# Kernel tuning notes

Measured on AMD Instinct MI355X. Metric: run time of the kernel, lower is better.

Reference implementation:

```python
import jax, jax.numpy as jnp
import numpy as np
from jax import lax

B, T = 64, 200
NUM_C, DIM_S, SIZE_M = 2000, 128, 50


def setup_inputs() -> dict:
    key = jax.random.key(0)
    ks = jax.random.split(key, 12)
    d = {}
    d['skill'] = jax.random.randint(ks[0], (B, T), 0, NUM_C)
    d['answer'] = jax.random.randint(ks[1], (B, T), 0, 2)
    s = 1.0 / np.sqrt(DIM_S)
    d['k_emb'] = jax.random.normal(ks[2], (NUM_C + 1, DIM_S), jnp.float32)
    d['v_emb'] = jax.random.normal(ks[3], (2 * NUM_C + 1, DIM_S), jnp.float32)
    # kaiming_normal on [size_m, dim_s]: std = sqrt(2/dim_s)
    d['Mk'] = jax.random.normal(ks[4], (SIZE_M, DIM_S), jnp.float32) * np.sqrt(2.0 / DIM_S)
    d['Mv0'] = jax.random.normal(ks[5], (SIZE_M, DIM_S), jnp.float32) * np.sqrt(2.0 / DIM_S)
    d['f_W'] = jax.random.normal(ks[6], (DIM_S, 2 * DIM_S), jnp.float32) * (1.0 / np.sqrt(2 * DIM_S))
    d['f_b'] = jnp.zeros((DIM_S,), jnp.float32)
    d['p_W'] = jax.random.normal(ks[7], (NUM_C, DIM_S), jnp.float32) * s
    d['p_b'] = jnp.zeros((NUM_C,), jnp.float32)
    d['e_W'] = jax.random.normal(ks[8], (DIM_S, DIM_S), jnp.float32) * s
    d['e_b'] = jnp.zeros((DIM_S,), jnp.float32)
    d['a_W'] = jax.random.normal(ks[9], (DIM_S, DIM_S), jnp.float32) * s
    d['a_b'] = jnp.zeros((DIM_S,), jnp.float32)
    return d


def reference(skill, answer, k_emb, v_emb, Mk, Mv0, f_W, f_b, p_W, p_b, e_W, e_b, a_W, a_b):
    num_c = p_W.shape[0]
    bsz = skill.shape[0]
    answer_x = jnp.where(answer == 2, 1, answer)
    x = skill + num_c * answer_x                       # [B,T]
    k = k_emb[skill]                                   # [B,T,D]
    v = v_emb[x]                                       # [B,T,D]
    w = jax.nn.softmax(jnp.einsum('btd,md->btm', k, Mk), axis=-1)   # [B,T,M]
    e = jax.nn.sigmoid(jnp.einsum('btd,ed->bte', v, e_W) + e_b)      # [B,T,D]
    a = jnp.tanh(jnp.einsum('btd,ed->bte', v, a_W) + a_b)            # [B,T,D]

    Mv_init = jnp.broadcast_to(Mv0, (bsz,) + Mv0.shape)              # [B,M,D]

    def step(Mvt, inp):
        et, at, wt = inp                               # [B,D],[B,D],[B,M]
        # read uses pre-update memory (Mv[:, :-1] in the torch code)
        read = jnp.einsum('bm,bmd->bd', wt, Mvt)
        Mvt_new = Mvt * (1.0 - wt[:, :, None] * et[:, None, :]) + wt[:, :, None] * at[:, None, :]
        return Mvt_new, read

    _, reads = lax.scan(step, Mv_init,
                        (e.transpose(1, 0, 2), a.transpose(1, 0, 2), w.transpose(1, 0, 2)))
    reads = reads.transpose(1, 0, 2)                   # [B,T,D]

    f = jnp.tanh(jnp.concatenate([reads, k], axis=-1) @ f_W.T + f_b)  # [B,T,D]
    p = jax.nn.sigmoid(f @ p_W.T + p_b)                # [B,T,num_c] (dropout is identity at eval)
    p = p[:, :-1, :]
    next_skill = skill[:, 1:]                          # [B,T-1]
    idx = jnp.minimum(next_skill, num_c - 1)
    pred = jnp.take_along_axis(p, idx[..., None], axis=-1)[..., 0]
    pred = jnp.where(next_skill < num_c, pred, 0.0)    # index num_c -> zero row in torch one_hot
    return pred
```

## Files before the change

kernel.cpp:

```cpp
#include <hip/hip_runtime.h>
#include <math.h>

#define Bsz 64
#define Tn 200
#define NUMC 2000
#define DS 128
#define SM 50
#define NTOK (Bsz*Tn)
#define WG2 10
#define MPG2 5

typedef __attribute__((ext_vector_type(8))) short bfrag;
typedef __attribute__((ext_vector_type(4))) float f32x4;
typedef __attribute__((ext_vector_type(2))) float f32x2;
typedef __attribute__((ext_vector_type(4))) unsigned int u32x4;

__device__ __forceinline__ unsigned short f2bf(float x) {
    unsigned int u = __builtin_bit_cast(unsigned int, x);
    u = u + 0x7fffu + ((u >> 16) & 1u);
    return (unsigned short)(u >> 16);
}
__device__ __forceinline__ unsigned int pack2(float a, float b) {
    return (unsigned int)f2bf(a) | ((unsigned int)f2bf(b) << 16);
}
__device__ __forceinline__ bfrag mk_frag(f32x4 x, f32x4 y) {
    u32x4 t;
    t[0] = pack2(x[0], x[1]); t[1] = pack2(x[2], x[3]);
    t[2] = pack2(y[0], y[1]); t[3] = pack2(y[2], y[3]);
    return __builtin_bit_cast(bfrag, t);
}

__device__ __forceinline__ float fast_exp(float x)  { return __builtin_amdgcn_exp2f(x * 1.44269504f); }
__device__ __forceinline__ float fast_rcp(float x)  { return __builtin_amdgcn_rcpf(x); }
__device__ __forceinline__ float fast_sigmoid(float x) { return fast_rcp(1.f + fast_exp(-x)); }
__device__ __forceinline__ float fast_tanh(float x) { return 1.f - 2.f * fast_rcp(fast_exp(2.f * x) + 1.f); }

__device__ __forceinline__ void load_group(const bfrag* __restrict__ B, int nt0, int L, bfrag bf[4][4]) {
    #pragma unroll
    for (int t = 0; t < 4; t++)
        #pragma unroll
        for (int ki = 0; ki < 4; ki++)
            bf[t][ki] = B[(size_t)((nt0 + t) * 4 + ki) * 64 + L];
}
__device__ __forceinline__ void mfma_group(const bfrag A[4], const bfrag bf[4][4], f32x4 acc[4]) {
    #pragma unroll
    for (int ki = 0; ki < 4; ki++)
        #pragma unroll
        for (int t = 0; t < 4; t++)
            acc[t] = __builtin_amdgcn_mfma_f32_16x16x32_bf16(A[ki], bf[t][ki], acc[t], 0, 0, 0);
}

__global__ __launch_bounds__(256) void k0_cast(
    const float* __restrict__ eW, const float* __restrict__ aW,
    const float* __restrict__ fW, const float* __restrict__ Mk,
    unsigned int* __restrict__ BeaU, unsigned int* __restrict__ BkmU,
    unsigned int* __restrict__ Bf0U)
{
    const int g = blockIdx.x * 256 + threadIdx.x;
    if (g >= 9216) return;
    int gm, mat;
    unsigned int* dst;
    if (g < 4096)      { mat = 0; gm = g;        dst = BeaU; }
    else if (g < 7168) { mat = 1; gm = g - 4096; dst = BkmU; }
    else               { mat = 2; gm = g - 7168; dst = Bf0U; }
    const int nt = gm >> 8, r = gm & 255, ki = r >> 6, L = r & 63;
    const int n = nt * 16 + (L & 15);
    const int k = ki * 32 + (L >> 4) * 8;

    const float* src = nullptr;
    if (mat == 0) {
        src = (n < 128) ? (eW + (size_t)n * DS + k) : (aW + (size_t)(n - 128) * DS + k);
    } else if (mat == 1) {
        if (n < 128)           src = fW + (size_t)n * (2 * DS) + DS + k;
        else if (n < 128 + SM) src = Mk + (size_t)(n - 128) * DS + k;
    } else {
        src = fW + (size_t)n * (2 * DS) + k;
    }
    float v[8];
    #pragma unroll
    for (int j = 0; j < 8; j++) v[j] = src ? src[j] : 0.f;
    u32x4 o;
    o[0] = pack2(v[0], v[1]); o[1] = pack2(v[2], v[3]);
    o[2] = pack2(v[4], v[5]); o[3] = pack2(v[6], v[7]);
    ((u32x4*)dst)[gm] = o;
}

__global__ __launch_bounds__(64) void k1_gemm(
    const int* __restrict__ skill, const int* __restrict__ answer,
    const float* __restrict__ k_emb, const float* __restrict__ v_emb,
    const unsigned int* __restrict__ BeaU, const unsigned int* __restrict__ BkmU,
    const float* __restrict__ eB, const float* __restrict__ aB,
    float* __restrict__ w2, float* __restrict__ ea_buf, float* __restrict__ kp_buf)
{
    const int bid = blockIdx.x;
    const int L = threadIdx.x, L15 = L & 15, quad = L >> 4;

    if (bid < NTOK/16) {
        const int tok0 = bid * 16;
        const int tokA = tok0 + L15;
        const int tokD0 = tok0 + quad * 4;

        const bfrag* Bea = (const bfrag*)BeaU;
        bfrag bfA[4][4], bfB[4][4];
        load_group(Bea, 0, L, bfA);
        load_group(Bea, 4, L, bfB);

        const int s  = skill[tokA];
        const int an = answer[tokA];
        const int ax = (an == 2) ? 1 : an;
        const float* vp = v_emb + ((size_t)(s + NUMC * ax)) * DS + quad * 8;
        bfrag Vf[4];
        #pragma unroll
        for (int ki = 0; ki < 4; ki++) {
            const f32x4* a = (const f32x4*)(vp + ki * 32);
            Vf[ki] = mk_frag(a[0], a[1]);
        }

        f32x4 acc[4];
        #pragma unroll
        for (int t = 0; t < 4; t++) acc[t] = (f32x4){0.f,0.f,0.f,0.f};
        mfma_group(Vf, bfA, acc);
        load_group(Bea, 8, L, bfA);
        #pragma unroll
        for (int t = 0; t < 4; t++) {
            const int n = t * 16 + L15;
            const float bias = eB[n];
            #pragma unroll
            for (int reg = 0; reg < 4; reg++)
                ea_buf[(size_t)(tokD0 + reg) * (2*DS) + 2*n] = fast_sigmoid(acc[t][reg] + bias);
        }

        #pragma unroll
        for (int t = 0; t < 4; t++) acc[t] = (f32x4){0.f,0.f,0.f,0.f};
        mfma_group(Vf, bfB, acc);
        load_group(Bea, 12, L, bfB);
        #pragma unroll
        for (int t = 0; t < 4; t++) {
            const int n = (4 + t) * 16 + L15;
            const float bias = eB[n];
            #pragma unroll
            for (int reg = 0; reg < 4; reg++)
                ea_buf[(size_t)(tokD0 + reg) * (2*DS) + 2*n] = fast_sigmoid(acc[t][reg] + bias);
        }

        #pragma unroll
        for (int t = 0; t < 4; t++) acc[t] = (f32x4){0.f,0.f,0.f,0.f};
        mfma_group(Vf, bfA, acc);
        #pragma unroll
        for (int t = 0; t < 4; t++) {
            const int n = t * 16 + L15;
            const float bias = aB[n];
            #pragma unroll
            for (int reg = 0; reg < 4; reg++)
                ea_buf[(size_t)(tokD0 + reg) * (2*DS) + 2*n + 1] = fast_tanh(acc[t][reg] + bias);
        }

        #pragma unroll
        for (int t = 0; t < 4; t++) acc[t] = (f32x4){0.f,0.f,0.f,0.f};
        mfma_group(Vf, bfB, acc);
        #pragma unroll
        for (int t = 0; t < 4; t++) {
            const int n = (4 + t) * 16 + L15;
            const float bias = aB[n];
            #pragma unroll
            for (int reg = 0; reg < 4; reg++)
                ea_buf[(size_t)(tokD0 + reg) * (2*DS) + 2*n + 1] = fast_tanh(acc[t][reg] + bias);
        }
    } else {
        const int tok0 = (bid - NTOK/16) * 16;
        const int tokA = tok0 + L15;
        const int tokD0 = tok0 + quad * 4;

        const bfrag* Bkm = (const bfrag*)BkmU;
        bfrag bfA[4][4], bfB[4][4];
        load_group(Bkm, 0, L, bfA);
        load_group(Bkm, 4, L, bfB);

        const int s = skill[tokA];
        const float* kp = k_emb + (size_t)s * DS + quad * 8;
        bfrag Kf[4];
        #pragma unroll
        for (int ki = 0; ki < 4; ki++) {
            const f32x4* b = (const f32x4*)(kp + ki * 32);
            Kf[ki] = mk_frag(b[0], b[1]);
        }

        f32x4 acc[4];
        #pragma unroll
        for (int t = 0; t < 4; t++) acc[t] = (f32x4){0.f,0.f,0.f,0.f};
        mfma_group(Kf, bfA, acc);
        load_group(Bkm, 8, L, bfA);
        #pragma unroll
        for (int t = 0; t < 4; t++) {
            const int n = t * 16 + L15;
            #pragma unroll
            for (int reg = 0; reg < 4; reg++)
                kp_buf[(size_t)(tokD0 + reg) * DS + n] = acc[t][reg];
        }

        #pragma unroll
        for (int t = 0; t < 4; t++) acc[t] = (f32x4){0.f,0.f,0.f,0.f};
        mfma_group(Kf, bfB, acc);
        #pragma unroll
        for (int t = 0; t < 4; t++) {
            const int n = (4 + t) * 16 + L15;
            #pragma unroll
            for (int reg = 0; reg < 4; reg++)
                kp_buf[(size_t)(tokD0 + reg) * DS + n] = acc[t][reg];
        }

        #pragma unroll
        for (int t = 0; t < 4; t++) acc[t] = (f32x4){0.f,0.f,0.f,0.f};
        mfma_group(Kf, bfA, acc);
        #pragma unroll
        for (int reg = 0; reg < 4; reg++) {
            float mx = -1e30f;
            #pragma unroll
            for (int t = 0; t < 4; t++) {
                const int c = t * 16 + L15;
                if (c < SM) mx = fmaxf(mx, acc[t][reg]);
            }
            #pragma unroll
            for (int msk = 1; msk <= 8; msk <<= 1)
                mx = fmaxf(mx, __shfl_xor(mx, msk));
            float ex[4], sum = 0.f;
            #pragma unroll
            for (int t = 0; t < 4; t++) {
                const int c = t * 16 + L15;
                ex[t] = (c < SM) ? fast_exp(acc[t][reg] - mx) : 0.f;
                sum += ex[t];
            }
            #pragma unroll
            for (int msk = 1; msk <= 8; msk <<= 1)
                sum += __shfl_xor(sum, msk);
            const float inv = fast_rcp(sum);
            float* wp = w2 + (size_t)(tok0 + quad * 4 + reg) * 80;
            #pragma unroll
            for (int t = 0; t < 4; t++) {
                const int c = t * 16 + L15;
                if (c < SM) wp[(c / MPG2) * 8 + (c % MPG2)] = ex[t] * inv;
            }
        }
    }
}

__global__ __launch_bounds__(64, 2) void k2_scan(
    const float* __restrict__ w2, const float* __restrict__ ea_buf,
    const float* __restrict__ Mv0, float* __restrict__ part_buf)
{
    const int bi   = blockIdx.x;
    const int b    = bi / (2*WG2);
    const int r    = bi % (2*WG2);
    const int dh   = r / WG2;
    const int mg   = r % WG2;
    const int lane = threadIdx.x;
    const int d    = dh*64 + lane;
    const int m0   = mg * MPG2;
    const int base = b * Tn;

    float Mv[MPG2];
    #pragma unroll
    for (int m = 0; m < MPG2; m++) Mv[m] = Mv0[(size_t)(m0+m)*DS + d];

    float* pout = part_buf + (size_t)mg * NTOK * DS;

    f32x2 rea[8][2];
    float rw[8][2][MPG2];

    #define LOADST(ST, T)                                                          \
        { const int tc_ = ((T) < Tn) ? (T) : 0;                                    \
          _Pragma("unroll")                                                        \
          for (int q_ = 0; q_ < 2; q_++) {                                         \
              const int tf_ = base + tc_ + q_;                                     \
              rea[ST][q_] = *(const f32x2*)(ea_buf + (size_t)tf_*(2*DS) + 2*d);    \
              const float* wp_ = w2 + (size_t)tf_*80 + mg*8;                       \
              f32x4 w4_ = *(const f32x4*)wp_;                                      \
              rw[ST][q_][0]=w4_[0]; rw[ST][q_][1]=w4_[1];                          \
              rw[ST][q_][2]=w4_[2]; rw[ST][q_][3]=w4_[3];                          \
              rw[ST][q_][4]=wp_[4];                                               \
          } }

    #define STAGE(ST, T0)                                                          \
        { _Pragma("unroll")                                                        \
          for (int q = 0; q < 2; q++) {                                            \
              const float ev = rea[ST][q][0], av = rea[ST][q][1];                  \
              float rd = 0.f;                                                      \
              _Pragma("unroll")                                                    \
              for (int m = 0; m < MPG2; m++) {                                     \
                  const float wm = rw[ST][q][m];                                   \
                  rd = fmaf(wm, Mv[m], rd);                            \
                  Mv[m] = fmaf(-wm, fmaf(ev, Mv[m], -av), Mv[m]);      \
              }                                                                    \
              pout[(size_t)(base + (T0) + q)*DS + d] = rd;                         \
          }                                                                        \
          LOADST(ST, (T0) + 16) }

    LOADST(0, 0) LOADST(1, 2) LOADST(2, 4) LOADST(3, 6)
    LOADST(4, 8) LOADST(5, 10) LOADST(6, 12) LOADST(7, 14)

    for (int blk = 0; blk < 12; blk++) {
        const int t0 = blk * 16;
        STAGE(0, t0)      STAGE(1, t0 + 2)  STAGE(2, t0 + 4)  STAGE(3, t0 + 6)
        STAGE(4, t0 + 8)  STAGE(5, t0 + 10) STAGE(6, t0 + 12) STAGE(7, t0 + 14)
    }
    STAGE(0, 192) STAGE(1, 194) STAGE(2, 196) STAGE(3, 198)
    #undef STAGE
    #undef LOADST
}

__global__ __launch_bounds__(64) void k3_gemm(
    const float* __restrict__ part_buf, const float* __restrict__ kp_buf,
    const unsigned int* __restrict__ Bf0U, const float* __restrict__ fB,
    const float* __restrict__ pW, const float* __restrict__ pB,
    const int* __restrict__ skill, float* __restrict__ out)
{
    const int L = threadIdx.x, L15 = L & 15, quad = L >> 4;
    const int tok0 = blockIdx.x * 16;
    const int tokA = tok0 + L15;
    const int tokD0 = tok0 + quad * 4;

    const bfrag* Bf0 = (const bfrag*)Bf0U;
    bfrag bfA[4][4], bfB[4][4];
    load_group(Bf0, 0, L, bfA);
    load_group(Bf0, 4, L, bfB);

    bfrag Rf[4];
    #pragma unroll
    for (int ki = 0; ki < 4; ki++) {
        const float* p0 = part_buf + (size_t)tokA * DS + ki * 32 + quad * 8;
        f32x4 x = (f32x4){0.f,0.f,0.f,0.f}, y = (f32x4){0.f,0.f,0.f,0.f};
        #pragma unroll
        for (int g = 0; g < WG2; g++) {
            const f32x4* q4 = (const f32x4*)(p0 + (size_t)g * NTOK * DS);
            x = x + q4[0]; y = y + q4[1];
        }
        Rf[ki] = mk_frag(x, y);
    }

    float f[4][8];
    f32x4 acc[4];

    #pragma unroll
    for (int t = 0; t < 4; t++) acc[t] = (f32x4){0.f,0.f,0.f,0.f};
    mfma_group(Rf, bfA, acc);
    #pragma unroll
    for (int t = 0; t < 4; t++) {
        const int n = t * 16 + L15;
        const float fb = fB[n];
        #pragma unroll
        for (int reg = 0; reg < 4; reg++)
            f[reg][t] = fast_tanh(acc[t][reg] + kp_buf[(size_t)(tokD0 + reg) * DS + n] + fb);
    }

    #pragma unroll
    for (int t = 0; t < 4; t++) acc[t] = (f32x4){0.f,0.f,0.f,0.f};
    mfma_group(Rf, bfB, acc);
    #pragma unroll
    for (int t = 0; t < 4; t++) {
        const int n = (4 + t) * 16 + L15;
        const float fb = fB[n];
        #pragma unroll
        for (int reg = 0; reg < 4; reg++)
            f[reg][4 + t] = fast_tanh(acc[t][reg] + kp_buf[(size_t)(tokD0 + reg) * DS + n] + fb);
    }

    #pragma unroll
    for (int reg = 0; reg < 4; reg++) {
        const int tok = tokD0 + reg;
        const int t = tok % Tn;
        const bool act = (t < Tn - 1);
        int sn = 0, ix = 0;
        float contrib = 0.f;
        if (act) {
            sn = skill[tok + 1];
            ix = (sn < NUMC) ? sn : (NUMC - 1);
            const float* pr = pW + (size_t)ix * DS + L15;
            #pragma unroll
            for (int nt = 0; nt < 8; nt++)
                contrib = fmaf(f[reg][nt], pr[nt * 16], contrib);
        }
        #pragma unroll
        for (int msk = 1; msk <= 8; msk <<= 1)
            contrib += __shfl_xor(contrib, msk);
        if (act && L15 == 0) {
            const float val = contrib + pB[ix];
            const float prd = (sn < NUMC) ? fast_sigmoid(val) : 0.f;
            out[(size_t)(tok / Tn) * (Tn - 1) + t] = prd;
        }
    }
}

extern "C" void kernel_launch(void* const* d_in, const int* in_sizes, int n_in,
                              void* d_out, int out_size, void* d_ws, size_t ws_size,
                              hipStream_t stream)
{
    const int*   skill  = (const int*)  d_in[0];
    const int*   answer = (const int*)  d_in[1];
    const float* k_emb  = (const float*)d_in[2];
    const float* v_emb  = (const float*)d_in[3];
    const float* Mk     = (const float*)d_in[4];
    const float* Mv0    = (const float*)d_in[5];
    const float* f_W    = (const float*)d_in[6];
    const float* f_b    = (const float*)d_in[7];
    const float* p_W    = (const float*)d_in[8];
    const float* p_b    = (const float*)d_in[9];
    const float* e_W    = (const float*)d_in[10];
    const float* e_b    = (const float*)d_in[11];
    const float* a_W    = (const float*)d_in[12];
    const float* a_b    = (const float*)d_in[13];
    float* out = (float*)d_out;

    float* ws       = (float*)d_ws;
    float* w2       = ws;
    float* ea_buf   = w2     + (size_t)NTOK*80;
    float* kp_buf   = ea_buf + (size_t)NTOK*2*DS;
    float* part_buf = kp_buf + (size_t)NTOK*DS;
    unsigned int* BeaU = (unsigned int*)(part_buf + (size_t)WG2*NTOK*DS);
    unsigned int* BkmU = BeaU + 4096 * 4;
    unsigned int* Bf0U = BkmU + 3072 * 4;

    k0_cast<<<36, 256, 0, stream>>>(e_W, a_W, f_W, Mk, BeaU, BkmU, Bf0U);
    k1_gemm<<<2*(NTOK/16), 64, 0, stream>>>(skill, answer, k_emb, v_emb,
        BeaU, BkmU, e_b, a_b, w2, ea_buf, kp_buf);
    k2_scan<<<Bsz*2*WG2, 64, 0, stream>>>(w2, ea_buf, Mv0, part_buf);
    k3_gemm<<<NTOK/16, 64, 0, stream>>>(part_buf, kp_buf, Bf0U, f_b,
        p_W, p_b, skill, out);
}
```

Measured before the change: 155.3 us.

## Store erase/add and partial reads in bf16 to halve intermediate traffic

The erase/add gate values are packed as two bf16s per 32-bit word instead of two floats, and the per-group partial read vectors written by the scan are stored as bf16 instead of fp32. This halves the bytes moving through the intermediate buffers between the three kernels, notably the ten partial read buffers that k3 sums. The k1 epilogue is also reorganised to compute all four MFMA groups up front before writing. The cost is lower precision on the memory-update inputs and on the partial sums, which could accumulate error across the 200-step recurrence.

Result: faster. 151.1 us (-2.7%).

```diff
diff --git a/kernel.cpp b/kernel.cpp
--- a/kernel.cpp
+++ b/kernel.cpp
@@ -12,7 +12,6 @@
 
 typedef __attribute__((ext_vector_type(8))) short bfrag;
 typedef __attribute__((ext_vector_type(4))) float f32x4;
-typedef __attribute__((ext_vector_type(2))) float f32x2;
 typedef __attribute__((ext_vector_type(4))) unsigned int u32x4;
 
 __device__ __forceinline__ unsigned short f2bf(float x) {
@@ -22,6 +21,9 @@
 }
 __device__ __forceinline__ unsigned int pack2(float a, float b) {
     return (unsigned int)f2bf(a) | ((unsigned int)f2bf(b) << 16);
+}
+__device__ __forceinline__ float bf2f(unsigned int u) {
+    return __builtin_bit_cast(float, u << 16);
 }
 __device__ __forceinline__ bfrag mk_frag(f32x4 x, f32x4 y) {
     u32x4 t;
@@ -90,7 +92,7 @@
     const float* __restrict__ k_emb, const float* __restrict__ v_emb,
     const unsigned int* __restrict__ BeaU, const unsigned int* __restrict__ BkmU,
     const float* __restrict__ eB, const float* __restrict__ aB,
-    float* __restrict__ w2, float* __restrict__ ea_buf, float* __restrict__ kp_buf)
+    float* __restrict__ w2, unsigned int* __restrict__ ea32, float* __restrict__ kp_buf)
 {
     const int bid = blockIdx.x;
     const int L = threadIdx.x, L15 = L & 15, quad = L >> 4;
@@ -116,55 +118,33 @@
             Vf[ki] = mk_frag(a[0], a[1]);
         }
 
-        f32x4 acc[4];
-        #pragma unroll
-        for (int t = 0; t < 4; t++) acc[t] = (f32x4){0.f,0.f,0.f,0.f};
-        mfma_group(Vf, bfA, acc);
+        f32x4 acc0[4], acc1[4], acc2[4], acc3[4];
+        #pragma unroll
+        for (int t = 0; t < 4; t++) {
+            acc0[t] = (f32x4){0.f,0.f,0.f,0.f}; acc1[t] = (f32x4){0.f,0.f,0.f,0.f};
+            acc2[t] = (f32x4){0.f,0.f,0.f,0.f}; acc3[t] = (f32x4){0.f,0.f,0.f,0.f};
+        }
+        mfma_group(Vf, bfA, acc0);
         load_group(Bea, 8, L, bfA);
+        mfma_group(Vf, bfB, acc1);
+        load_group(Bea, 12, L, bfB);
+        mfma_group(Vf, bfA, acc2);
+        mfma_group(Vf, bfB, acc3);
+
         #pragma unroll
         for (int t = 0; t < 4; t++) {
-            const int n = t * 16 + L15;
-            const float bias = eB[n];
-            #pragma unroll
-            for (int reg = 0; reg < 4; reg++)
-                ea_buf[(size_t)(tokD0 + reg) * (2*DS) + 2*n] = fast_sigmoid(acc[t][reg] + bias);
-        }
-
-        #pragma unroll
-        for (int t = 0; t < 4; t++) acc[t] = (f32x4){0.f,0.f,0.f,0.f};
-        mfma_group(Vf, bfB, acc);
-        load_group(Bea, 12, L, bfB);
-        #pragma unroll
-        for (int t = 0; t < 4; t++) {
-            const int n = (4 + t) * 16 + L15;
-            const float bias = eB[n];
-            #pragma unroll
-            for (int reg = 0; reg < 4; reg++)
-                ea_buf[(size_t)(tokD0 + reg) * (2*DS) + 2*n] = fast_sigmoid(acc[t][reg] + bias);
-        }
-
-        #pragma unroll
-        for (int t = 0; t < 4; t++) acc[t] = (f32x4){0.f,0.f,0.f,0.f};
-        mfma_group(Vf, bfA, acc);
-        #pragma unroll
-        for (int t = 0; t < 4; t++) {
-            const int n = t * 16 + L15;
-            const float bias = aB[n];
-            #pragma unroll
-            for (int reg = 0; reg < 4; reg++)
-                ea_buf[(size_t)(tokD0 + reg) * (2*DS) + 2*n + 1] = fast_tanh(acc[t][reg] + bias);
-        }
-
-        #pragma unroll
-        for (int t = 0; t < 4; t++) acc[t] = (f32x4){0.f,0.f,0.f,0.f};
-        mfma_group(Vf, bfB, acc);
-        #pragma unroll
-        for (int t = 0; t < 4; t++) {
-            const int n = (4 + t) * 16 + L15;
-            const float bias = aB[n];
-            #pragma unroll
-            for (int reg = 0; reg < 4; reg++)
-                ea_buf[(size_t)(tokD0 + reg) * (2*DS) + 2*n + 1] = fast_tanh(acc[t][reg] + bias);
+            const int n0 = t * 16 + L15;
+            const int n1 = n0 + 64;
+            const float eb0 = eB[n0], ab0 = aB[n0];
+            const float eb1 = eB[n1], ab1 = aB[n1];
+            #pragma unroll
+            for (int reg = 0; reg < 4; reg++) {
+                const size_t tok = (size_t)(tokD0 + reg);
+                ea32[tok * DS + n0] = pack2(fast_sigmoid(acc0[t][reg] + eb0),
+                                            fast_tanh   (acc2[t][reg] + ab0));
+                ea32[tok * DS + n1] = pack2(fast_sigmoid(acc1[t][reg] + eb1),
+                                            fast_tanh   (acc3[t][reg] + ab1));
+            }
         }
     } else {
         const int tok0 = (bid - NTOK/16) * 16;
@@ -245,8 +225,8 @@
 }
 
 __global__ __launch_bounds__(64, 2) void k2_scan(
-    const float* __restrict__ w2, const float* __restrict__ ea_buf,
-    const float* __restrict__ Mv0, float* __restrict__ part_buf)
+    const float* __restrict__ w2, const unsigned int* __restrict__ ea32,
+    const float* __restrict__ Mv0, unsigned short* __restrict__ part16)
 {
     const int bi   = blockIdx.x;
     const int b    = bi / (2*WG2);
@@ -262,9 +242,9 @@
     #pragma unroll
     for (int m = 0; m < MPG2; m++) Mv[m] = Mv0[(size_t)(m0+m)*DS + d];
 
-    float* pout = part_buf + (size_t)mg * NTOK * DS;
-
-    f32x2 rea[8][2];
+    unsigned short* pout = part16 + (size_t)mg * NTOK * DS;
+
+    unsigned int rea[8][2];
     float rw[8][2][MPG2];
 
     #define LOADST(ST, T)                                                          \
@@ -272,7 +252,7 @@
           _Pragma("unroll")                                                        \
           for (int q_ = 0; q_ < 2; q_++) {                                         \
               const int tf_ = base + tc_ + q_;                                     \
-              rea[ST][q_] = *(const f32x2*)(ea_buf + (size_t)tf_*(2*DS) + 2*d);    \
+              rea[ST][q_] = ea32[(size_t)tf_*DS + d];                              \
               const float* wp_ = w2 + (size_t)tf_*80 + mg*8;                       \
               f32x4 w4_ = *(const f32x4*)wp_;                                      \
               rw[ST][q_][0]=w4_[0]; rw[ST][q_][1]=w4_[1];                          \
@@ -283,7 +263,8 @@
     #define STAGE(ST, T0)                                                          \
         { _Pragma("unroll")                                                        \
           for (int q = 0; q < 2; q++) {                                            \
-              const float ev = rea[ST][q][0], av = rea[ST][q][1];                  \
+              const unsigned int v_ = rea[ST][q];                                  \
+              const float ev = bf2f(v_ & 0xffffu), av = bf2f(v_ >> 16);            \
               float rd = 0.f;                                                      \
               _Pragma("unroll")                                                    \
               for (int m = 0; m < MPG2; m++) {                                     \
@@ -291,7 +272,7 @@
                   rd = fmaf(wm, Mv[m], rd);                            \
                   Mv[m] = fmaf(-wm, fmaf(ev, Mv[m], -av), Mv[m]);      \
               }                                                                    \
-              pout[(size_t)(base + (T0) + q)*DS + d] = rd;                         \
+              pout[(size_t)(base + (T0) + q)*DS + d] = f2bf(rd);                   \
           }                                                                        \
           LOADST(ST, (T0) + 16) }
 
@@ -309,7 +290,7 @@
 }
 
 __global__ __launch_bounds__(64) void k3_gemm(
-    const float* __restrict__ part_buf, const float* __restrict__ kp_buf,
+    const unsigned short* __restrict__ part16, const float* __restrict__ kp_buf,
     const unsigned int* __restrict__ Bf0U, const float* __restrict__ fB,
     const float* __restrict__ pW, const float* __restrict__ pB,
     const int* __restrict__ skill, float* __restrict__ out)
@@ -327,14 +308,17 @@
     bfrag Rf[4];
     #pragma unroll
     for (int ki = 0; ki < 4; ki++) {
-        const float* p0 = part_buf + (size_t)tokA * DS + ki * 32 + quad * 8;
-        f32x4 x = (f32x4){0.f,0.f,0.f,0.f}, y = (f32x4){0.f,0.f,0.f,0.f};
+        const unsigned short* p0 = part16 + (size_t)tokA * DS + ki * 32 + quad * 8;
+        float s0=0,s1=0,s2=0,s3=0,s4=0,s5=0,s6=0,s7=0;
         #pragma unroll
         for (int g = 0; g < WG2; g++) {
-            const f32x4* q4 = (const f32x4*)(p0 + (size_t)g * NTOK * DS);
-            x = x + q4[0]; y = y + q4[1];
-        }
-        Rf[ki] = mk_frag(x, y);
+            u32x4 v = *(const u32x4*)(p0 + (size_t)g * NTOK * DS);
+            s0 += bf2f(v[0] & 0xffffu); s1 += bf2f(v[0] >> 16);
+            s2 += bf2f(v[1] & 0xffffu); s3 += bf2f(v[1] >> 16);
+            s4 += bf2f(v[2] & 0xffffu); s5 += bf2f(v[2] >> 16);
+            s6 += bf2f(v[3] & 0xffffu); s7 += bf2f(v[3] >> 16);
+        }
+        Rf[ki] = mk_frag((f32x4){s0,s1,s2,s3}, (f32x4){s4,s5,s6,s7});
     }
 
     float f[4][8];
@@ -410,19 +394,19 @@
     const float* a_b    = (const float*)d_in[13];
     float* out = (float*)d_out;
 
-    float* ws       = (float*)d_ws;
-    float* w2       = ws;
-    float* ea_buf   = w2     + (size_t)NTOK*80;
-    float* kp_buf   = ea_buf + (size_t)NTOK*2*DS;
-    float* part_buf = kp_buf + (size_t)NTOK*DS;
-    unsigned int* BeaU = (unsigned int*)(part_buf + (size_t)WG2*NTOK*DS);
+    float* ws     = (float*)d_ws;
+    float* w2     = ws;
+    unsigned int* ea32 = (unsigned int*)(w2 + (size_t)NTOK*80);
+    float* kp_buf = (float*)(ea32 + (size_t)NTOK*DS);
+    unsigned short* part16 = (unsigned short*)(kp_buf + (size_t)NTOK*DS);
+    unsigned int* BeaU = (unsigned int*)(part16 + (size_t)WG2*NTOK*DS);
     unsigned int* BkmU = BeaU + 4096 * 4;
     unsigned int* Bf0U = BkmU + 3072 * 4;
 
     k0_cast<<<36, 256, 0, stream>>>(e_W, a_W, f_W, Mk, BeaU, BkmU, Bf0U);
     k1_gemm<<<2*(NTOK/16), 64, 0, stream>>>(skill, answer, k_emb, v_emb,
-        BeaU, BkmU, e_b, a_b, w2, ea_buf, kp_buf);
-    k2_scan<<<Bsz*2*WG2, 64, 0, stream>>>(w2, ea_buf, Mv0, part_buf);
-    k3_gemm<<<NTOK/16, 64, 0, stream>>>(part_buf, kp_buf, Bf0U, f_b,
+        BeaU, BkmU, e_b, a_b, w2, ea32, kp_buf);
+    k2_scan<<<Bsz*2*WG2, 64, 0, stream>>>(w2, ea32, Mv0, part16);
+    k3_gemm<<<NTOK/16, 64, 0, stream>>>(part16, kp_buf, Bf0U, f_b,
         p_W, p_b, skill, out);
 }
```
